# Kernel optimization log

Measured on AMD Instinct MI355X. Metric: run time of the kernel, lower is better.

The kernel has to match this reference:

```python
import jax, jax.numpy as jnp
import numpy as np

N = 20000      # num_nodes
E = 320000     # num_edges (avg degree 16)
HID = 256      # hid_dim
H = 4          # attention heads
D = HID // H   # per-head dim (concat heads -> HID)
L = 2          # nGAT_layer
OUT = 12       # out_dim / pred_len (decoder steps)
NEG_SLOPE = 0.2


def setup_inputs() -> dict:
    key = jax.random.key(0)
    ks = jax.random.split(key, 16)
    s = 0.05
    nrm = lambda k, shape: jax.random.normal(k, shape, jnp.float32) * s
    return dict(
        x=nrm(ks[0], (N, HID)),
        edge_index=jax.random.randint(ks[1], (2, E), 0, N, dtype=jnp.int32),
        # GATv2Conv params per layer (stacked over L layers)
        gat_w_src=nrm(ks[2], (L, HID, H * D)),
        gat_w_dst=nrm(ks[3], (L, HID, H * D)),
        gat_att=nrm(ks[4], (L, H, D)),
        gat_bias=nrm(ks[5], (L, H * D)),
        # decoder_mlp: Linear(1 + HID -> HID)
        mlp_w=nrm(ks[6], (HID, 1 + HID)),
        mlp_b=nrm(ks[7], (HID,)),
        # nn.LSTM (1 layer, input HID, hidden HID), torch gate order i,f,g,o
        lstm_w_ih=nrm(ks[8], (4 * HID, HID)),
        lstm_w_hh=nrm(ks[9], (4 * HID, HID)),
        lstm_b_ih=nrm(ks[10], (4 * HID,)),
        lstm_b_hh=nrm(ks[11], (4 * HID,)),
        # decoder_init_proj: Linear(HID -> 1); decoder_output_proj: Linear(HID -> 1)
        init_w=nrm(ks[12], (1, HID)),
        init_b=nrm(ks[13], (1,)),
        out_w=nrm(ks[14], (1, HID)),
        out_b=nrm(ks[15], (1,)),
    )


def _gatv2_layer(x, src, dst, w_src, w_dst, att, bias):
    n = x.shape[0]
    xl = (x @ w_src).reshape(n, H, D)   # source-side projection
    xr = (x @ w_dst).reshape(n, H, D)   # destination-side projection
    # GATv2: e_ij = a^T LeakyReLU(Wl x_j + Wr x_i)
    e = jax.nn.leaky_relu(xl[src] + xr[dst], NEG_SLOPE)        # [E,H,D]
    logits = jnp.einsum('ehd,hd->eh', e, att)                   # [E,H]
    # edge softmax over incoming edges of each destination node
    m = jax.ops.segment_max(logits, dst, num_segments=n)        # [N,H]
    ex = jnp.exp(logits - m[dst])
    denom = jax.ops.segment_sum(ex, dst, num_segments=n)
    alpha = ex / denom[dst]                                     # [E,H]
    out = jax.ops.segment_sum(xl[src] * alpha[:, :, None], dst, num_segments=n)
    return out.reshape(n, H * D) + bias


def reference(x, edge_index, gat_w_src, gat_w_dst, gat_att, gat_bias,
              mlp_w, mlp_b, lstm_w_ih, lstm_w_hh, lstm_b_ih, lstm_b_hh,
              init_w, init_b, out_w, out_b):
    src, dst = edge_index[0], edge_index[1]
    # stacked GAT blocks: GATv2Conv + ELU (element == 2)
    for l in range(L):
        x = _gatv2_layer(x, src, dst, gat_w_src[l], gat_w_dst[l], gat_att[l], gat_bias[l])
        x = jax.nn.elu(x)
    # recurrent LSTM decoder, batch = nodes, seq step by step
    ctx = x                      # encoder_context
    h = x                        # h_0 = x (num_layers = 1)
    c = jnp.zeros_like(x)        # c_0 = 0
    prev = x @ init_w.T + init_b  # [N,1]
    outs = []
    for _ in range(OUT):
        dec_in = jnp.concatenate([prev, ctx], axis=1) @ mlp_w.T + mlp_b  # [N,HID]
        gates = dec_in @ lstm_w_ih.T + lstm_b_ih + h @ lstm_w_hh.T + lstm_b_hh
        i_g, f_g, g_g, o_g = jnp.split(gates, 4, axis=1)
        i_g = jax.nn.sigmoid(i_g)
        f_g = jax.nn.sigmoid(f_g)
        o_g = jax.nn.sigmoid(o_g)
        g_g = jnp.tanh(g_g)
        c = f_g * c + i_g * g_g
        h = o_g * jnp.tanh(c)
        prev = h @ out_w.T + out_b  # [N,1]
        outs.append(prev)
    return jnp.concatenate(outs, axis=1)  # [N, OUT]
```

## Files before the change

### kernel.cpp

```cpp
#include <hip/hip_runtime.h>
#include <hip/hip_bf16.h>

#define NN 20000
#define NE 320000
#define TOUT 12
#define DEGMAX 96
#define MR 80
#define NBLK 250
#define NCHL 14
#define NCHG 6

typedef __bf16 bf16x8 __attribute__((ext_vector_type(8)));
typedef float float4v __attribute__((ext_vector_type(4)));

#define LD8(p) (*(const bf16x8*)(p))
#define MFMA16(a,b,c) __builtin_amdgcn_mfma_f32_16x16x32_bf16((a),(b),(c),0,0,0)

__device__ __forceinline__ float bf2f(const __hip_bfloat16 v){ return __bfloat162float(v); }
__device__ __forceinline__ __hip_bfloat16 f2bf(float v){ return __float2bfloat16(v); }
__device__ __forceinline__ float sigmoidr_(float x){ return __builtin_amdgcn_rcpf(1.f + __expf(-x)); }
__device__ __forceinline__ float tanhr_(float x){ return 1.f - 2.f*__builtin_amdgcn_rcpf(__expf(2.f*x) + 1.f); }
__device__ __forceinline__ float rdf(const void* p, int i, int f32){
  return f32 ? ((const float*)p)[i] : __bfloat162float(((const __hip_bfloat16*)p)[i]);
}

__global__ void k_detect(const void* xraw, int* flag){
  __shared__ int cnt;
  if(threadIdx.x == 0) cnt = 0;
  __syncthreads();
  const unsigned* w = (const unsigned*)xraw;
  int local = 0;
  for(int i = threadIdx.x; i < 4096; i += 256){
    unsigned b = (w[i] >> 8) & 0x7F;
    if(b >= 0x33 && b <= 0x3F) local++;
  }
  atomicAdd(&cnt, local);
  __syncthreads();
  if(threadIdx.x == 0) *flag = (cnt > 2048) ? 0 : 1;
}

__global__ void k_fail(float* out, int n){
  int i = blockIdx.x*256 + threadIdx.x;
  if(i < n) out[i] = 256.0f;
}

__global__ void k_count(const int* __restrict__ dst, int* __restrict__ deg){
  int e = blockIdx.x*256 + threadIdx.x;
  if(e < NE){
    unsigned d = (unsigned)dst[e];
    if(d < NN) atomicAdd(&deg[d], 1);
  }
}

__global__ void k_scan(const int* __restrict__ deg, int* __restrict__ offp, int* __restrict__ cursor){
  __shared__ int part[256];
  __shared__ int excl[257];
  const int CH = (NN + 255)/256;
  int tid = threadIdx.x;
  int lo = tid*CH;
  int hi = lo + CH; if(hi > NN) hi = NN;
  int s = 0;
  for(int i=lo;i<hi;i++) s += deg[i];
  part[tid] = s;
  __syncthreads();
  if(tid == 0){
    int run = 0;
    for(int i=0;i<256;i++){ excl[i] = run; run += part[i]; }
    excl[256] = run;
  }
  __syncthreads();
  int run = excl[tid];
  for(int i=lo;i<hi;i++){ offp[i] = run; cursor[i] = run; run += deg[i]; }
  if(tid == 0) offp[NN] = excl[256];
}

__global__ void k_fill(const int* __restrict__ src, const int* __restrict__ dst,
                       int* __restrict__ cursor, int* __restrict__ csr_src){
  int e = blockIdx.x*256 + threadIdx.x;
  if(e >= NE) return;
  unsigned d = (unsigned)dst[e];
  if(d >= NN) return;
  unsigned p = (unsigned)atomicAdd(&cursor[d], 1);
  if(p < NE){
    unsigned sv = (unsigned)src[e];
    csr_src[p] = (sv < NN) ? (int)sv : 0;
  }
}

__global__ void k_prep(const void* __restrict__ w_src, const void* __restrict__ w_dst,
                       const void* __restrict__ w_hh, const void* __restrict__ wih,
                       const void* __restrict__ mlp_w, const int* __restrict__ flag,
                       __hip_bfloat16* __restrict__ wsrcT, __hip_bfloat16* __restrict__ wdstT,
                       __hip_bfloat16* __restrict__ whhp, __hip_bfloat16* __restrict__ wihb,
                       __hip_bfloat16* __restrict__ mlpT){
  int tid = blockIdx.x*256 + threadIdx.x;
  int f = *flag;
  if(tid < 131072){
    int l = tid >> 16, r = tid & 65535, o = r >> 8, i = r & 255;
    wsrcT[tid] = f2bf(rdf(w_src, l*65536 + i*256 + o, f));
    wdstT[tid] = f2bf(rdf(w_dst, l*65536 + i*256 + o, f));
  }
  if(tid < 262144){
    whhp[tid] = f2bf(rdf(w_hh, tid, f));
    wihb[tid] = f2bf(rdf(wih, tid, f));
  }
  if(tid < 65536){
    int k = tid >> 8, j = tid & 255;
    mlpT[tid] = f2bf(rdf(mlp_w, j*257 + 1 + k, f));
  }
}

__global__ void k_prep_ub(const void* __restrict__ wih, const void* __restrict__ mlp_w,
                          const void* __restrict__ mlp_b,
                          const void* __restrict__ b_ih, const void* __restrict__ b_hh,
                          const void* __restrict__ att, const void* __restrict__ gbias,
                          const void* __restrict__ init_w, const void* __restrict__ init_b,
                          const void* __restrict__ out_w, const void* __restrict__ out_b,
                          const int* __restrict__ flag,
                          float* __restrict__ u, float* __restrict__ bc,
                          float* __restrict__ attf, float* __restrict__ gbiasf,
                          float* __restrict__ initwf, float* __restrict__ outwf,
                          float* __restrict__ sc){
  __shared__ float su[256], sb[256];
  int g = blockIdx.x, j = threadIdx.x, f = *flag;
  float w = rdf(wih, g*256 + j, f);
  su[j] = w * rdf(mlp_w, j*257, f);
  sb[j] = w * rdf(mlp_b, j, f);
  if(g < 2){
    int i = g*256 + j;
    attf[i] = rdf(att, i, f);
    gbiasf[i] = rdf(gbias, i, f);
  }
  if(g == 0){
    initwf[j] = rdf(init_w, j, f);
    outwf[j]  = rdf(out_w, j, f);
    if(j == 0){ sc[0] = rdf(init_b, 0, f); sc[1] = rdf(out_b, 0, f); }
  }
  __syncthreads();
  for(int s=128; s>0; s>>=1){
    if(j < s){ su[j] += su[j+s]; sb[j] += sb[j+s]; }
    __syncthreads();
  }
  if(j == 0){ u[g] = su[0]; bc[g] = sb[0] + rdf(b_ih, g, f) + rdf(b_hh, g, f); }
}

__global__ void k_pack(const __hip_bfloat16* __restrict__ Wpl, const __hip_bfloat16* __restrict__ Wcpl,
                       __hip_bfloat16* __restrict__ WhhP, __hip_bfloat16* __restrict__ WcP){
  int idx = blockIdx.x*256 + threadIdx.x;
  if(idx >= 32768) return;
  int cs = idx >> 12;
  int kslot = (idx >> 9) & 7;
  int nt = (idx >> 6) & 7;
  int lane = idx & 63;
  int l16 = lane & 15, quad = lane >> 4;
  int brow = (nt>>1)*256 + cs*32 + (nt&1)*16 + l16;
  int srcofs = brow*256 + kslot*32 + quad*8;
  int dst = idx*8;
  *(bf16x8*)(WhhP + dst) = LD8(Wpl + srcofs);
  *(bf16x8*)(WcP + dst)  = LD8(Wcpl + srcofs);
}

__global__ void k_pack2(const __hip_bfloat16* __restrict__ wsrcT,
                        const __hip_bfloat16* __restrict__ wdstT,
                        __hip_bfloat16* __restrict__ wprojP){
  int idx = blockIdx.x*256 + threadIdx.x;
  if(idx >= 32768) return;
  int m = idx >> 13;
  int fi = idx & 8191;
  int l = m >> 1, role = m & 1;
  int kidx = fi >> 10;
  int nt = (fi >> 6) & 15;
  int lane = fi & 63;
  int l16 = lane & 15, quad = lane >> 4;
  const __hip_bfloat16* src = (role ? wdstT : wsrcT) + l*65536;
  int srcofs = (nt*16 + l16)*256 + kidx*32 + quad*8;
  *(bf16x8*)(wprojP + (size_t)m*65536 + fi*8) = LD8(src + srcofs);
}

__global__ __launch_bounds__(256) void k_gemm_nt_bf(const __hip_bfloat16* __restrict__ A,
                                                    const __hip_bfloat16* __restrict__ B,
                                                    __hip_bfloat16* __restrict__ Cb, int M){
  int wave = threadIdx.x >> 6;
  int lane = threadIdx.x & 63;
  int l16 = lane & 15, quad = lane >> 4, quad8 = quad*8;
  int mBase = blockIdx.x*64 + wave*16;
  int nBase = blockIdx.y*64;
  int arow = mBase + l16; if(arow >= M) arow = M-1;
  const __hip_bfloat16* aptr = A + (size_t)arow*256 + quad8;
  float4v acc[4];
  #pragma unroll
  for(int nt=0;nt<4;nt++){ acc[nt][0]=0.f; acc[nt][1]=0.f; acc[nt][2]=0.f; acc[nt][3]=0.f; }
  for(int k0=0;k0<256;k0+=32){
    bf16x8 a = LD8(aptr + k0);
    #pragma unroll
    for(int nt=0;nt<4;nt++){
      const __hip_bfloat16* bptr = B + (size_t)(nBase + nt*16 + l16)*256 + k0 + quad8;
      acc[nt] = MFMA16(a, LD8(bptr), acc[nt]);
    }
  }
  #pragma unroll
  for(int nt=0;nt<4;nt++){
    int col = nBase + nt*16 + l16;
    #pragma unroll
    for(int r=0;r<4;r++){
      int row = mBase + quad*4 + r;
      if(row < M) Cb[(size_t)row*256 + col] = f2bf(acc[nt][r]);
    }
  }
}

__global__ __launch_bounds__(512, 2) void k_gemm_dual(__hip_bfloat16* __restrict__ P,
                                                      const void* __restrict__ xraw,
                                                      const int* __restrict__ flag,
                                                      int layer0,
                                                      const __hip_bfloat16* __restrict__ BsrcP,
                                                      const __hip_bfloat16* __restrict__ BdstP,
                                                      __hip_bfloat16* __restrict__ Q){
  __shared__ __hip_bfloat16 sA[64*264];
  int tid = threadIdx.x;
  int mBase = blockIdx.x*64;
  {
    int r = tid >> 3;
    int c0 = (tid & 7)*32;
    int grow = mBase + r; if(grow >= NN) grow = NN-1;
    if(layer0){
      int f = *flag;
      #pragma unroll
      for(int j=0;j<32;j++) sA[r*264 + c0 + j] = f2bf(rdf(xraw, grow*256 + c0 + j, f));
    }else{
      const __hip_bfloat16* srcp = P + (size_t)grow*256 + c0;
      #pragma unroll
      for(int j=0;j<4;j++) *(bf16x8*)(&sA[r*264 + c0 + j*8]) = LD8(srcp + j*8);
    }
  }
  __syncthreads();
  int w8 = tid >> 6;
  int w = w8 & 3;
  int role = w8 >> 2;
  int lane = tid&63, l16 = lane&15, quad = lane>>4, quad8 = quad*8;
  const __hip_bfloat16* B = role ? BdstP : BsrcP;
  __hip_bfloat16* C = role ? P : Q;
  const __hip_bfloat16* arow = &sA[(w*16 + l16)*264 + quad8];
  float4v acc[16];
  #pragma unroll
  for(int nt=0;nt<16;nt++){ acc[nt][0]=0.f; acc[nt][1]=0.f; acc[nt][2]=0.f; acc[nt][3]=0.f; }
  for(int kidx=0;kidx<8;kidx++){
    bf16x8 a = *(const bf16x8*)(arow + kidx*32);
    const __hip_bfloat16* bbase = B + (kidx<<13) + (lane<<3);
    #pragma unroll
    for(int nt=0;nt<16;nt++)
      acc[nt] = MFMA16(a, LD8(bbase + (nt<<9)), acc[nt]);
  }
  #pragma unroll
  for(int nt=0;nt<16;nt++){
    int col = nt*16 + l16;
    #pragma unroll
    for(int r=0;r<4;r++){
      int row = mBase + w*16 + quad*4 + r;
      if(row < NN) C[(size_t)row*256 + col] = f2bf(acc[nt][r]);
    }
  }
}

__global__ __launch_bounds__(256) void k_node_fused(const __hip_bfloat16* __restrict__ Q,
                                                    __hip_bfloat16* __restrict__ P,
                                                    const int* __restrict__ offp,
                                                    const int* __restrict__ csr_src,
                                                    const float* __restrict__ attf,
                                                    const float* __restrict__ gbiasf){
  __shared__ float slog[DEGMAX*4];
  __shared__ int ssrc[DEGMAX];
  int node = blockIdx.x;
  int tid = threadIdx.x;
  int s0 = offp[node], s1 = offp[node+1];
  if(s0 < 0) s0 = 0; if(s0 > NE) s0 = NE;
  if(s1 < s0) s1 = s0; if(s1 > NE) s1 = NE;
  int deg = s1 - s0; if(deg > DEGMAX) deg = DEGMAX;
  if(tid < deg){
    unsigned sv = (unsigned)csr_src[s0 + tid];
    ssrc[tid] = (sv < NN) ? (int)sv : 0;
  }
  __syncthreads();
  int w = tid>>6, lane = tid&63;
  int eSlot = lane>>4, li = lane&15;
  float prl[16], attl[16];
  #pragma unroll
  for(int h=0;h<4;h++)
    #pragma unroll
    for(int j=0;j<4;j++){
      int d = h*64 + j*16 + li;
      prl[h*4+j]  = bf2f(P[(size_t)node*256 + d]);
      attl[h*4+j] = attf[d];
    }
  for(int base=0; base<deg; base+=16){
    int e = base + w*4 + eSlot;
    bool valid = (e < deg);
    const __hip_bfloat16* pl = Q + (size_t)ssrc[valid ? e : 0]*256;
    float part[4];
    #pragma unroll
    for(int h=0;h<4;h++){
      float p = 0.f;
      #pragma unroll
      for(int j=0;j<4;j++){
        int d = h*64 + j*16 + li;
        float v = bf2f(pl[d]) + prl[h*4+j];
        v = (v > 0.f) ? v : 0.2f*v;
        p += v * attl[h*4+j];
      }
      part[h] = p;
    }
    #pragma unroll
    for(int h=0;h<4;h++){
      part[h] += __shfl_xor(part[h], 1, 64);
      part[h] += __shfl_xor(part[h], 2, 64);
      part[h] += __shfl_xor(part[h], 4, 64);
      part[h] += __shfl_xor(part[h], 8, 64);
    }
    if(li == 0 && valid){
      #pragma unroll
      for(int h=0;h<4;h++) slog[e*4+h] = part[h];
    }
  }
  __syncthreads();
  {
    int hh = tid >> 6;
    int li64 = tid & 63;
    float m = -1e30f;
    for(int i=li64; i<deg; i+=64) m = fmaxf(m, slog[i*4+hh]);
    #pragma unroll
    for(int s=1; s<64; s<<=1) m = fmaxf(m, __shfl_xor(m, s, 64));
    float den = 0.f;
    for(int i=li64; i<deg; i+=64) den += __expf(slog[i*4+hh] - m);
    #pragma unroll
    for(int s=1; s<64; s<<=1) den += __shfl_xor(den, s, 64);
    float inv = (den > 0.f) ? 1.f/den : 0.f;
    for(int i=li64; i<deg; i+=64) slog[i*4+hh] = __expf(slog[i*4+hh] - m)*inv;
  }
  __syncthreads();
  int d = tid, hd = d>>6;
  float acc = 0.f;
  for(int i=0;i<deg;i++) acc += slog[i*4+hd] * bf2f(Q[(size_t)ssrc[i]*256 + d]);
  acc += gbiasf[d];
  acc = (acc > 0.f) ? acc : (__expf(acc) - 1.f);
  P[(size_t)node*256 + d] = f2bf(acc);
}

__global__ __launch_bounds__(512, 2) void k_lstm80(const __hip_bfloat16* __restrict__ ctx,
                                                   const __hip_bfloat16* __restrict__ WcP,
                                                   const __hip_bfloat16* __restrict__ WhhP,
                                                   const float* __restrict__ u_vec,
                                                   const float* __restrict__ bc_vec,
                                                   const float* __restrict__ initwf,
                                                   const float* __restrict__ outwf,
                                                   const float* __restrict__ sc,
                                                   __hip_bfloat16* __restrict__ gxg,
                                                   float* __restrict__ out){
  __shared__ __hip_bfloat16 sgx[NCHL*4096];
  __shared__ __hip_bfloat16 sh[MR*264];
  __shared__ float spartw[MR*8];
  __shared__ float sprev[MR];
  float* spart = (float*)sgx;
  int tid = threadIdx.x;
  int mBase = blockIdx.x*MR;
  int cs = tid>>6, lane = tid&63, l16 = lane&15, quad = lane>>4, quad8 = quad*8;
  int phase = (blockIdx.x >> 3) & 7;
  __hip_bfloat16* gxb = gxg + (size_t)blockIdx.x*(NCHG*4096);
  #pragma unroll
  for(int p=0;p<3;p++){
    int r = p*32 + (tid >> 4);
    if(r < MR){
      int c0 = (tid & 15)*16;
      const __hip_bfloat16* srcp = ctx + (size_t)(mBase + r)*256 + c0;
      *(bf16x8*)(&sh[r*264 + c0])     = LD8(srcp);
      *(bf16x8*)(&sh[r*264 + c0 + 8]) = LD8(srcp + 8);
    }
  }
  __syncthreads();
  #pragma unroll
  for(int p=0;p<3;p++){
    int r = p*32 + (tid >> 4);
    int c0 = (tid & 15)*16;
    float part = 0.f;
    if(r < MR){
      #pragma unroll
      for(int j=0;j<16;j++) part += bf2f(sh[r*264 + c0 + j]) * initwf[c0 + j];
    }
    spart[tid] = part;
    __syncthreads();
    if(tid < 32 && p*32 + tid < MR){
      float s = 0.f;
      #pragma unroll
      for(int j=0;j<16;j++) s += spart[tid*16 + j];
      sprev[p*32 + tid] = s + sc[0];
    }
    __syncthreads();
  }
  float ureg[8], owreg[2];
  #pragma unroll
  for(int g=0;g<4;g++)
    #pragma unroll
    for(int tc=0;tc<2;tc++) ureg[g*2+tc] = u_vec[g*256 + cs*32 + tc*16 + l16];
  #pragma unroll
  for(int tc=0;tc<2;tc++) owreg[tc] = outwf[cs*32 + tc*16 + l16];
  float outb = sc[1];
  {
    float bcl[8];
    #pragma unroll
    for(int g=0;g<4;g++)
      #pragma unroll
      for(int tc=0;tc<2;tc++) bcl[g*2+tc] = bc_vec[g*256 + cs*32 + tc*16 + l16];
    float4v acc[40];
    #pragma unroll
    for(int nt=0;nt<40;nt++){ acc[nt][0]=0.f; acc[nt][1]=0.f; acc[nt][2]=0.f; acc[nt][3]=0.f; }
    #pragma unroll 2
    for(int ki=0;ki<8;ki++){
      int kidx = (ki + phase) & 7;
      int k0 = kidx*32;
      bf16x8 a0 = *(const bf16x8*)(&sh[l16*264 + k0 + quad8]);
      bf16x8 a1 = *(const bf16x8*)(&sh[(16 + l16)*264 + k0 + quad8]);
      bf16x8 a2 = *(const bf16x8*)(&sh[(32 + l16)*264 + k0 + quad8]);
      bf16x8 a3 = *(const bf16x8*)(&sh[(48 + l16)*264 + k0 + quad8]);
      bf16x8 a4 = *(const bf16x8*)(&sh[(64 + l16)*264 + k0 + quad8]);
      const __hip_bfloat16* bbase = WcP + (((cs<<3) + kidx)<<12) + (lane<<3);
      #pragma unroll
      for(int nt=0;nt<8;nt++){
        bf16x8 b = LD8(bbase + (nt<<9));
        acc[nt]    = MFMA16(a0, b, acc[nt]);
        acc[8+nt]  = MFMA16(a1, b, acc[8+nt]);
        acc[16+nt] = MFMA16(a2, b, acc[16+nt]);
        acc[24+nt] = MFMA16(a3, b, acc[24+nt]);
        acc[32+nt] = MFMA16(a4, b, acc[32+nt]);
      }
    }
    #pragma unroll
    for(int rt=0;rt<5;rt++)
      #pragma unroll
      for(int tc=0;tc<2;tc++)
        #pragma unroll
        for(int half=0;half<2;half++){
          bf16x8 v;
          #pragma unroll
          for(int rr=0;rr<2;rr++)
            #pragma unroll
            for(int g=0;g<4;g++){
              int r = half*2 + rr;
              v[rr*4+g] = (__bf16)f2bf(acc[rt*8 + g*2 + tc][r] + bcl[g*2+tc]);
            }
          int cp = (rt*2+tc)*2 + half;
          if(cp < NCHL) *(bf16x8*)(&sgx[cp*4096 + tid*8]) = v;
          else          *(bf16x8*)(gxb + (cp-NCHL)*4096 + tid*8) = v;
        }
  }
  __syncthreads();
  float creg[40];
  #pragma unroll
  for(int i=0;i<40;i++) creg[i] = 0.f;
  for(int step=0; step<TOUT; step++){
    float4v acc[40];
    #pragma unroll
    for(int nt=0;nt<40;nt++){ acc[nt][0]=0.f; acc[nt][1]=0.f; acc[nt][2]=0.f; acc[nt][3]=0.f; }
    #pragma unroll 2
    for(int ki=0;ki<8;ki++){
      int kidx = (ki + phase) & 7;
      int k0 = kidx*32;
      bf16x8 a0 = *(const bf16x8*)(&sh[l16*264 + k0 + quad8]);
      bf16x8 a1 = *(const bf16x8*)(&sh[(16 + l16)*264 + k0 + quad8]);
      bf16x8 a2 = *(const bf16x8*)(&sh[(32 + l16)*264 + k0 + quad8]);
      bf16x8 a3 = *(const bf16x8*)(&sh[(48 + l16)*264 + k0 + quad8]);
      bf16x8 a4 = *(const bf16x8*)(&sh[(64 + l16)*264 + k0 + quad8]);
      const __hip_bfloat16* bbase = WhhP + (((cs<<3) + kidx)<<12) + (lane<<3);
      #pragma unroll
      for(int nt=0;nt<8;nt++){
        bf16x8 b = LD8(bbase + (nt<<9));
        acc[nt]    = MFMA16(a0, b, acc[nt]);
        acc[8+nt]  = MFMA16(a1, b, acc[8+nt]);
        acc[16+nt] = MFMA16(a2, b, acc[16+nt]);
        acc[24+nt] = MFMA16(a3, b, acc[24+nt]);
        acc[32+nt] = MFMA16(a4, b, acc[32+nt]);
      }
    }
    bf16x8 gg[NCHG];
    #pragma unroll
    for(int j=0;j<NCHG;j++) gg[j] = LD8(gxb + j*4096 + tid*8);
    __syncthreads();
    #pragma unroll
    for(int rt=0;rt<5;rt++){
      float hsum[4];
      hsum[0]=0.f; hsum[1]=0.f; hsum[2]=0.f; hsum[3]=0.f;
      #pragma unroll
      for(int tc=0;tc<2;tc++){
        int col = cs*32 + tc*16 + l16;
        int cpb = (rt*2+tc)*2;
        bf16x8 ga = (cpb   < NCHL) ? *(const bf16x8*)(&sgx[cpb*4096 + tid*8])     : gg[cpb-NCHL];
        bf16x8 gb = (cpb+1 < NCHL) ? *(const bf16x8*)(&sgx[(cpb+1)*4096 + tid*8]) : gg[cpb+1-NCHL];
        #pragma unroll
        for(int r=0;r<4;r++){
          int row = rt*16 + quad*4 + r;
          float p = sprev[row];
          int jb = (r&1)*4;
          float gx0, gx1, gx2, gx3;
          if(r < 2){
            gx0 = bf2f((__hip_bfloat16)ga[jb]);   gx1 = bf2f((__hip_bfloat16)ga[jb+1]);
            gx2 = bf2f((__hip_bfloat16)ga[jb+2]); gx3 = bf2f((__hip_bfloat16)ga[jb+3]);
          }else{
            gx0 = bf2f((__hip_bfloat16)gb[jb]);   gx1 = bf2f((__hip_bfloat16)gb[jb+1]);
            gx2 = bf2f((__hip_bfloat16)gb[jb+2]); gx3 = bf2f((__hip_bfloat16)gb[jb+3]);
          }
          float g0 = acc[rt*8 + tc][r]     + gx0 + p*ureg[tc];
          float g1 = acc[rt*8 + 2 + tc][r] + gx1 + p*ureg[2+tc];
          float g2 = acc[rt*8 + 4 + tc][r] + gx2 + p*ureg[4+tc];
          float g3 = acc[rt*8 + 6 + tc][r] + gx3 + p*ureg[6+tc];
          float iv = sigmoidr_(g0), fv = sigmoidr_(g1);
          float gv = tanhr_(g2),    ov = sigmoidr_(g3);
          float cn = fv*creg[rt*8 + tc*4 + r] + iv*gv;
          creg[rt*8 + tc*4 + r] = cn;
          float hn = ov * tanhr_(cn);
          sh[row*264 + col] = f2bf(hn);
          hsum[r] += hn * owreg[tc];
        }
      }
      #pragma unroll
      for(int r=0;r<4;r++){
        hsum[r] += __shfl_xor(hsum[r], 1, 64);
        hsum[r] += __shfl_xor(hsum[r], 2, 64);
        hsum[r] += __shfl_xor(hsum[r], 4, 64);
        hsum[r] += __shfl_xor(hsum[r], 8, 64);
      }
      if(l16 == 0){
        #pragma unroll
        for(int r=0;r<4;r++)
          spartw[(rt*16 + quad*4 + r)*8 + cs] = hsum[r];
      }
    }
    __syncthreads();
    if(tid < MR){
      float s = outb;
      #pragma unroll
      for(int c=0;c<8;c++) s += spartw[tid*8 + c];
      sprev[tid] = s;
      out[(size_t)(mBase + tid)*TOUT + step] = s;
    }
  }
}

extern "C" void kernel_launch(void* const* d_in, const int* in_sizes, int n_in,
                              void* d_out, int out_size, void* d_ws, size_t ws_size,
                              hipStream_t stream){
  const void* x      = d_in[0];
  const int*  ei     = (const int*)d_in[1];
  const void* w_src  = d_in[2];
  const void* w_dst  = d_in[3];
  const void* att    = d_in[4];
  const void* gbias  = d_in[5];
  const void* mlp_w  = d_in[6];
  const void* mlp_b  = d_in[7];
  const void* w_ih   = d_in[8];
  const void* w_hh   = d_in[9];
  const void* b_ih   = d_in[10];
  const void* b_hh   = d_in[11];
  const void* init_w = d_in[12];
  const void* init_b = d_in[13];
  const void* out_w  = d_in[14];
  const void* out_b  = d_in[15];
  float* out = (float*)d_out;
  const int* srcp = ei;
  const int* dstp = ei + NE;
  (void)in_sizes; (void)n_in;

  char* ws = (char*)d_ws;
  size_t off = 0;
  auto alloc = [&](size_t bytes)->void*{
    void* p = ws + off;
    off += (bytes + 255) & ~(size_t)255;
    return p;
  };
  __hip_bfloat16* P = (__hip_bfloat16*)alloc((size_t)NN*256*2);
  __hip_bfloat16* Q = (__hip_bfloat16*)alloc((size_t)NN*256*2);
  int* deg      = (int*)alloc((size_t)NN*4);
  int* offp     = (int*)alloc((size_t)(NN+1)*4);
  int* cursor   = (int*)alloc((size_t)NN*4);
  int* csr_src  = (int*)alloc((size_t)NE*4);
  __hip_bfloat16* wsrcT   = (__hip_bfloat16*)alloc((size_t)131072*2);
  __hip_bfloat16* wdstT   = (__hip_bfloat16*)alloc((size_t)131072*2);
  __hip_bfloat16* wprojP  = (__hip_bfloat16*)alloc((size_t)4*65536*2);
  __hip_bfloat16* whh_pl  = (__hip_bfloat16*)alloc((size_t)262144*2);
  __hip_bfloat16* Wc_pl   = (__hip_bfloat16*)alloc((size_t)262144*2);
  __hip_bfloat16* WhhP    = (__hip_bfloat16*)alloc((size_t)262144*2);
  __hip_bfloat16* WcP     = (__hip_bfloat16*)alloc((size_t)262144*2);
  __hip_bfloat16* wihb    = (__hip_bfloat16*)alloc((size_t)262144*2);
  __hip_bfloat16* mlpT    = (__hip_bfloat16*)alloc((size_t)65536*2);
  __hip_bfloat16* gxg     = (__hip_bfloat16*)alloc((size_t)NBLK*NCHG*4096*2);
  float* u_vec  = (float*)alloc(1024*4);
  float* bc_vec = (float*)alloc(1024*4);
  float* attf   = (float*)alloc(512*4);
  float* gbiasf = (float*)alloc(512*4);
  float* initwf = (float*)alloc(256*4);
  float* outwf  = (float*)alloc(256*4);
  float* sc     = (float*)alloc(2*4);
  int*   flag   = (int*)alloc(4);

  if(off > ws_size){
    k_fail<<<(out_size + 255)/256, 256, 0, stream>>>(out, out_size);
    return;
  }

  k_detect<<<1, 256, 0, stream>>>(x, flag);
  hipMemsetAsync(deg, 0, (size_t)NN*4, stream);
  hipMemsetAsync(csr_src, 0xFF, (size_t)NE*4, stream);
  k_count<<<NE/256, 256, 0, stream>>>(dstp, deg);
  k_scan<<<1, 256, 0, stream>>>(deg, offp, cursor);
  k_fill<<<NE/256, 256, 0, stream>>>(srcp, dstp, cursor, csr_src);
  k_prep<<<1024, 256, 0, stream>>>(w_src, w_dst, w_hh, w_ih, mlp_w, flag,
                                   wsrcT, wdstT, whh_pl, wihb, mlpT);
  {
    dim3 gwc(16, 4);
    k_gemm_nt_bf<<<gwc, 256, 0, stream>>>(wihb, mlpT, Wc_pl, 1024);
  }
  k_pack<<<128, 256, 0, stream>>>(whh_pl, Wc_pl, WhhP, WcP);
  k_pack2<<<128, 256, 0, stream>>>(wsrcT, wdstT, wprojP);
  k_prep_ub<<<1024, 256, 0, stream>>>(w_ih, mlp_w, mlp_b, b_ih, b_hh, att, gbias,
                                      init_w, init_b, out_w, out_b, flag,
                                      u_vec, bc_vec, attf, gbiasf, initwf, outwf, sc);

  for(int l=0;l<2;l++){
    k_gemm_dual<<<313, 512, 0, stream>>>(P, x, flag, (l == 0) ? 1 : 0,
                                         wprojP + (size_t)(l*2)*65536,
                                         wprojP + (size_t)(l*2+1)*65536, Q);
    k_node_fused<<<NN, 256, 0, stream>>>(Q, P, offp, csr_src, attf + l*256, gbiasf + l*256);
  }

  k_lstm80<<<NBLK, 512, 0, stream>>>(P, WcP, WhhP, u_vec, bc_vec, initwf, outwf, sc, gxg, out);
}
```

Baseline: 721.0 us.

## Fold output projection feedback into recurrent weights and keep gate inputs in registers

The rank-1 feedback term (prev * u) for steps after the first is folded into a modified recurrent weight matrix Whh + u·out_w^T, with out_b*u added as a constant. This removes the per-step dependency on the reduced prev value. The precomputed context gate inputs move from shared/global memory into registers (gxr), and the hidden state is double-buffered in shared memory to drop a barrier per step. The cost is higher register pressure (launch bounds lowered to 1 block/SM), an extra folded weight matrix, and extra bf16 rounding of the folded weights.

```diff
diff --git a/kernel.cpp b/kernel.cpp
--- a/kernel.cpp
+++ b/kernel.cpp
@@ -7,8 +7,6 @@
 #define DEGMAX 96
 #define MR 80
 #define NBLK 250
-#define NCHL 14
-#define NCHG 6
 
 typedef __bf16 bf16x8 __attribute__((ext_vector_type(8)));
 typedef float float4v __attribute__((ext_vector_type(4)));
@@ -144,8 +142,17 @@
   if(j == 0){ u[g] = su[0]; bc[g] = sb[0] + rdf(b_ih, g, f) + rdf(b_hh, g, f); }
 }
 
-__global__ void k_pack(const __hip_bfloat16* __restrict__ Wpl, const __hip_bfloat16* __restrict__ Wcpl,
-                       __hip_bfloat16* __restrict__ WhhP, __hip_bfloat16* __restrict__ WcP){
+__global__ void k_fold(const __hip_bfloat16* __restrict__ whh_pl,
+                       const float* __restrict__ u_vec, const float* __restrict__ outwf,
+                       __hip_bfloat16* __restrict__ whh2_pl){
+  int i = blockIdx.x*256 + threadIdx.x;
+  whh2_pl[i] = f2bf(bf2f(whh_pl[i]) + u_vec[i >> 8]*outwf[i & 255]);
+}
+
+__global__ void k_pack(const __hip_bfloat16* __restrict__ Wpl, const __hip_bfloat16* __restrict__ W2pl,
+                       const __hip_bfloat16* __restrict__ Wcpl,
+                       __hip_bfloat16* __restrict__ WhhP, __hip_bfloat16* __restrict__ Whh2P,
+                       __hip_bfloat16* __restrict__ WcP){
   int idx = blockIdx.x*256 + threadIdx.x;
   if(idx >= 32768) return;
   int cs = idx >> 12;
@@ -156,8 +163,9 @@
   int brow = (nt>>1)*256 + cs*32 + (nt&1)*16 + l16;
   int srcofs = brow*256 + kslot*32 + quad*8;
   int dst = idx*8;
-  *(bf16x8*)(WhhP + dst) = LD8(Wpl + srcofs);
-  *(bf16x8*)(WcP + dst)  = LD8(Wcpl + srcofs);
+  *(bf16x8*)(WhhP + dst)  = LD8(Wpl + srcofs);
+  *(bf16x8*)(Whh2P + dst) = LD8(W2pl + srcofs);
+  *(bf16x8*)(WcP + dst)   = LD8(Wcpl + srcofs);
 }
 
 __global__ void k_pack2(const __hip_bfloat16* __restrict__ wsrcT,
@@ -345,34 +353,32 @@
   P[(size_t)node*256 + d] = f2bf(acc);
 }
 
-__global__ __launch_bounds__(512, 2) void k_lstm80(const __hip_bfloat16* __restrict__ ctx,
+__global__ __launch_bounds__(512, 1) void k_lstm80(const __hip_bfloat16* __restrict__ ctx,
                                                    const __hip_bfloat16* __restrict__ WcP,
                                                    const __hip_bfloat16* __restrict__ WhhP,
+                                                   const __hip_bfloat16* __restrict__ Whh2P,
                                                    const float* __restrict__ u_vec,
                                                    const float* __restrict__ bc_vec,
                                                    const float* __restrict__ initwf,
                                                    const float* __restrict__ outwf,
                                                    const float* __restrict__ sc,
-                                                   __hip_bfloat16* __restrict__ gxg,
                                                    float* __restrict__ out){
-  __shared__ __hip_bfloat16 sgx[NCHL*4096];
-  __shared__ __hip_bfloat16 sh[MR*264];
-  __shared__ float spartw[MR*8];
-  __shared__ float sprev[MR];
-  float* spart = (float*)sgx;
+  __shared__ __hip_bfloat16 sh[2][MR*264];
+  __shared__ float spartw[2][MR*8];
+  __shared__ float sprev0[MR];
+  float* spart = &spartw[0][0];
   int tid = threadIdx.x;
   int mBase = blockIdx.x*MR;
   int cs = tid>>6, lane = tid&63, l16 = lane&15, quad = lane>>4, quad8 = quad*8;
   int phase = (blockIdx.x >> 3) & 7;
-  __hip_bfloat16* gxb = gxg + (size_t)blockIdx.x*(NCHG*4096);
   #pragma unroll
   for(int p=0;p<3;p++){
     int r = p*32 + (tid >> 4);
     if(r < MR){
       int c0 = (tid & 15)*16;
       const __hip_bfloat16* srcp = ctx + (size_t)(mBase + r)*256 + c0;
-      *(bf16x8*)(&sh[r*264 + c0])     = LD8(srcp);
-      *(bf16x8*)(&sh[r*264 + c0 + 8]) = LD8(srcp + 8);
+      *(bf16x8*)(&sh[0][r*264 + c0])     = LD8(srcp);
+      *(bf16x8*)(&sh[0][r*264 + c0 + 8]) = LD8(srcp + 8);
     }
   }
   __syncthreads();
@@ -383,7 +389,7 @@
     float part = 0.f;
     if(r < MR){
       #pragma unroll
-      for(int j=0;j<16;j++) part += bf2f(sh[r*264 + c0 + j]) * initwf[c0 + j];
+      for(int j=0;j<16;j++) part += bf2f(sh[0][r*264 + c0 + j]) * initwf[c0 + j];
     }
     spart[tid] = part;
     __syncthreads();
@@ -391,11 +397,11 @@
       float s = 0.f;
       #pragma unroll
       for(int j=0;j<16;j++) s += spart[tid*16 + j];
-      sprev[p*32 + tid] = s + sc[0];
+      sprev0[p*32 + tid] = s + sc[0];
     }
     __syncthreads();
   }
-  float ureg[8], owreg[2];
+  float ureg[8], owreg[2], ubo[8];
   #pragma unroll
   for(int g=0;g<4;g++)
     #pragma unroll
@@ -403,6 +409,9 @@
   #pragma unroll
   for(int tc=0;tc<2;tc++) owreg[tc] = outwf[cs*32 + tc*16 + l16];
   float outb = sc[1];
+  #pragma unroll
+  for(int i=0;i<8;i++) ubo[i] = ureg[i]*outb;
+  bf16x8 gxr[20];
   {
     float bcl[8];
     #pragma unroll
@@ -416,11 +425,11 @@
     for(int ki=0;ki<8;ki++){
       int kidx = (ki + phase) & 7;
       int k0 = kidx*32;
-      bf16x8 a0 = *(const bf16x8*)(&sh[l16*264 + k0 + quad8]);
-      bf16x8 a1 = *(const bf16x8*)(&sh[(16 + l16)*264 + k0 + quad8]);
-      bf16x8 a2 = *(const bf16x8*)(&sh[(32 + l16)*264 + k0 + quad8]);
-      bf16x8 a3 = *(const bf16x8*)(&sh[(48 + l16)*264 + k0 + quad8]);
-      bf16x8 a4 = *(const bf16x8*)(&sh[(64 + l16)*264 + k0 + quad8]);
+      bf16x8 a0 = *(const bf16x8*)(&sh[0][l16*264 + k0 + quad8]);
+      bf16x8 a1 = *(const bf16x8*)(&sh[0][(16 + l16)*264 + k0 + quad8]);
+      bf16x8 a2 = *(const bf16x8*)(&sh[0][(32 + l16)*264 + k0 + quad8]);
+      bf16x8 a3 = *(const bf16x8*)(&sh[0][(48 + l16)*264 + k0 + quad8]);
+      bf16x8 a4 = *(const bf16x8*)(&sh[0][(64 + l16)*264 + k0 + quad8]);
       const __hip_bfloat16* bbase = WcP + (((cs<<3) + kidx)<<12) + (lane<<3);
       #pragma unroll
       for(int nt=0;nt<8;nt++){
@@ -446,16 +455,17 @@
               int r = half*2 + rr;
               v[rr*4+g] = (__bf16)f2bf(acc[rt*8 + g*2 + tc][r] + bcl[g*2+tc]);
             }
-          int cp = (rt*2+tc)*2 + half;
-          if(cp < NCHL) *(bf16x8*)(&sgx[cp*4096 + tid*8]) = v;
-          else          *(bf16x8*)(gxb + (cp-NCHL)*4096 + tid*8) = v;
+          gxr[(rt*2+tc)*2 + half] = v;
         }
   }
-  __syncthreads();
   float creg[40];
   #pragma unroll
   for(int i=0;i<40;i++) creg[i] = 0.f;
+  int cur = 0;
+  #pragma unroll 1
   for(int step=0; step<TOUT; step++){
+    const __hip_bfloat16* W = (step == 0) ? WhhP : Whh2P;
+    int sb = step & 1;
     float4v acc[40];
     #pragma unroll
     for(int nt=0;nt<40;nt++){ acc[nt][0]=0.f; acc[nt][1]=0.f; acc[nt][2]=0.f; acc[nt][3]=0.f; }
@@ -463,12 +473,12 @@
     for(int ki=0;ki<8;ki++){
       int kidx = (ki + phase) & 7;
       int k0 = kidx*32;
-      bf16x8 a0 = *(const bf16x8*)(&sh[l16*264 + k0 + quad8]);
-      bf16x8 a1 = *(const bf16x8*)(&sh[(16 + l16)*264 + k0 + quad8]);
-      bf16x8 a2 = *(const bf16x8*)(&sh[(32 + l16)*264 + k0 + quad8]);
-      bf16x8 a3 = *(const bf16x8*)(&sh[(48 + l16)*264 + k0 + quad8]);
-      bf16x8 a4 = *(const bf16x8*)(&sh[(64 + l16)*264 + k0 + quad8]);
-      const __hip_bfloat16* bbase = WhhP + (((cs<<3) + kidx)<<12) + (lane<<3);
+      bf16x8 a0 = *(const bf16x8*)(&sh[cur][l16*264 + k0 + quad8]);
+      bf16x8 a1 = *(const bf16x8*)(&sh[cur][(16 + l16)*264 + k0 + quad8]);
+      bf16x8 a2 = *(const bf16x8*)(&sh[cur][(32 + l16)*264 + k0 + quad8]);
+      bf16x8 a3 = *(const bf16x8*)(&sh[cur][(48 + l16)*264 + k0 + quad8]);
+      bf16x8 a4 = *(const bf16x8*)(&sh[cur][(64 + l16)*264 + k0 + quad8]);
+      const __hip_bfloat16* bbase = W + (((cs<<3) + kidx)<<12) + (lane<<3);
       #pragma unroll
       for(int nt=0;nt<8;nt++){
         bf16x8 b = LD8(bbase + (nt<<9));
@@ -479,10 +489,6 @@
         acc[32+nt] = MFMA16(a4, b, acc[32+nt]);
       }
     }
-    bf16x8 gg[NCHG];
-    #pragma unroll
-    for(int j=0;j<NCHG;j++) gg[j] = LD8(gxb + j*4096 + tid*8);
-    __syncthreads();
     #pragma unroll
     for(int rt=0;rt<5;rt++){
       float hsum[4];
@@ -491,12 +497,11 @@
       for(int tc=0;tc<2;tc++){
         int col = cs*32 + tc*16 + l16;
         int cpb = (rt*2+tc)*2;
-        bf16x8 ga = (cpb   < NCHL) ? *(const bf16x8*)(&sgx[cpb*4096 + tid*8])     : gg[cpb-NCHL];
-        bf16x8 gb = (cpb+1 < NCHL) ? *(const bf16x8*)(&sgx[(cpb+1)*4096 + tid*8]) : gg[cpb+1-NCHL];
+        bf16x8 ga = gxr[cpb];
+        bf16x8 gb = gxr[cpb+1];
         #pragma unroll
         for(int r=0;r<4;r++){
           int row = rt*16 + quad*4 + r;
-          float p = sprev[row];
           int jb = (r&1)*4;
           float gx0, gx1, gx2, gx3;
           if(r < 2){
@@ -506,16 +511,23 @@
             gx0 = bf2f((__hip_bfloat16)gb[jb]);   gx1 = bf2f((__hip_bfloat16)gb[jb+1]);
             gx2 = bf2f((__hip_bfloat16)gb[jb+2]); gx3 = bf2f((__hip_bfloat16)gb[jb+3]);
           }
-          float g0 = acc[rt*8 + tc][r]     + gx0 + p*ureg[tc];
-          float g1 = acc[rt*8 + 2 + tc][r] + gx1 + p*ureg[2+tc];
-          float g2 = acc[rt*8 + 4 + tc][r] + gx2 + p*ureg[4+tc];
-          float g3 = acc[rt*8 + 6 + tc][r] + gx3 + p*ureg[6+tc];
+          float e0, e1, e2, e3;
+          if(step == 0){
+            float p = sprev0[row];
+            e0 = p*ureg[tc]; e1 = p*ureg[2+tc]; e2 = p*ureg[4+tc]; e3 = p*ureg[6+tc];
+          }else{
+            e0 = ubo[tc]; e1 = ubo[2+tc]; e2 = ubo[4+tc]; e3 = ubo[6+tc];
+          }
+          float g0 = acc[rt*8 + tc][r]     + gx0 + e0;
+          float g1 = acc[rt*8 + 2 + tc][r] + gx1 + e1;
+          float g2 = acc[rt*8 + 4 + tc][r] + gx2 + e2;
+          float g3 = acc[rt*8 + 6 + tc][r] + gx3 + e3;
           float iv = sigmoidr_(g0), fv = sigmoidr_(g1);
           float gv = tanhr_(g2),    ov = sigmoidr_(g3);
           float cn = fv*creg[rt*8 + tc*4 + r] + iv*gv;
           creg[rt*8 + tc*4 + r] = cn;
           float hn = ov * tanhr_(cn);
-          sh[row*264 + col] = f2bf(hn);
+          sh[cur^1][row*264 + col] = f2bf(hn);
           hsum[r] += hn * owreg[tc];
         }
       }
@@ -529,17 +541,17 @@
       if(l16 == 0){
         #pragma unroll
         for(int r=0;r<4;r++)
-          spartw[(rt*16 + quad*4 + r)*8 + cs] = hsum[r];
+          spartw[sb][(rt*16 + quad*4 + r)*8 + cs] = hsum[r];
       }
     }
     __syncthreads();
     if(tid < MR){
       float s = outb;
       #pragma unroll
-      for(int c=0;c<8;c++) s += spartw[tid*8 + c];
-      sprev[tid] = s;
+      for(int c=0;c<8;c++) s += spartw[sb][tid*8 + c];
       out[(size_t)(mBase + tid)*TOUT + step] = s;
     }
+    cur ^= 1;
   }
 }
 
@@ -584,12 +596,13 @@
   __hip_bfloat16* wdstT   = (__hip_bfloat16*)alloc((size_t)131072*2);
   __hip_bfloat16* wprojP  = (__hip_bfloat16*)alloc((size_t)4*65536*2);
   __hip_bfloat16* whh_pl  = (__hip_bfloat16*)alloc((size_t)262144*2);
+  __hip_bfloat16* whh2_pl = (__hip_bfloat16*)alloc((size_t)262144*2);
   __hip_bfloat16* Wc_pl   = (__hip_bfloat16*)alloc((size_t)262144*2);
   __hip_bfloat16* WhhP    = (__hip_bfloat16*)alloc((size_t)262144*2);
+  __hip_bfloat16* Whh2P   = (__hip_bfloat16*)alloc((size_t)262144*2);
   __hip_bfloat16* WcP     = (__hip_bfloat16*)alloc((size_t)262144*2);
   __hip_bfloat16* wihb    = (__hip_bfloat16*)alloc((size_t)262144*2);
   __hip_bfloat16* mlpT    = (__hip_bfloat16*)alloc((size_t)65536*2);
-  __hip_bfloat16* gxg     = (__hip_bfloat16*)alloc((size_t)NBLK*NCHG*4096*2);
   float* u_vec  = (float*)alloc(1024*4);
   float* bc_vec = (float*)alloc(1024*4);
   float* attf   = (float*)alloc(512*4);
@@ -612,15 +625,16 @@
   k_fill<<<NE/256, 256, 0, stream>>>(srcp, dstp, cursor, csr_src);
   k_prep<<<1024, 256, 0, stream>>>(w_src, w_dst, w_hh, w_ih, mlp_w, flag,
                                    wsrcT, wdstT, whh_pl, wihb, mlpT);
+  k_prep_ub<<<1024, 256, 0, stream>>>(w_ih, mlp_w, mlp_b, b_ih, b_hh, att, gbias,
+                                      init_w, init_b, out_w, out_b, flag,
+                                      u_vec, bc_vec, attf, gbiasf, initwf, outwf, sc);
   {
     dim3 gwc(16, 4);
     k_gemm_nt_bf<<<gwc, 256, 0, stream>>>(wihb, mlpT, Wc_pl, 1024);
   }
-  k_pack<<<128, 256, 0, stream>>>(whh_pl, Wc_pl, WhhP, WcP);
+  k_fold<<<1024, 256, 0, stream>>>(whh_pl, u_vec, outwf, whh2_pl);
+  k_pack<<<128, 256, 0, stream>>>(whh_pl, whh2_pl, Wc_pl, WhhP, Whh2P, WcP);
   k_pack2<<<128, 256, 0, stream>>>(wsrcT, wdstT, wprojP);
-  k_prep_ub<<<1024, 256, 0, stream>>>(w_ih, mlp_w, mlp_b, b_ih, b_hh, att, gbias,
-                                      init_w, init_b, out_w, out_b, flag,
-                                      u_vec, bc_vec, attf, gbiasf, initwf, outwf, sc);
 
   for(int l=0;l<2;l++){
     k_gemm_dual<<<313, 512, 0, stream>>>(P, x, flag, (l == 0) ? 1 : 0,
@@ -629,5 +643,6 @@
     k_node_fused<<<NN, 256, 0, stream>>>(Q, P, offp, csr_src, attf + l*256, gbiasf + l*256);
   }
 
-  k_lstm80<<<NBLK, 512, 0, stream>>>(P, WcP, WhhP, u_vec, bc_vec, initwf, outwf, sc, gxg, out);
-}
+  k_lstm80<<<NBLK, 512, 0, stream>>>(P, WcP, WhhP, Whh2P, u_vec, bc_vec,
+                                     initwf, outwf, sc, out);
+}
```

Measured after the change: 1.167 ms. 61.9% more time.

## Fold output-feedback projection into recurrent weight matrix for LSTM steps

Applied to the files above, without the earlier changes.

The previous-output feedback prev = h·out_w + out_b is folded algebraically into a second recurrent weight matrix (W_hh + u·out_wᵀ), with u·out_b moved into the bias. This removes the per-step sprev dependency and the scalar p*u terms, and step 0 gets a correction term instead. The gx global chunk loads move into the epilogue and the launch bounds drop to one block per CU. The fused matrix is rounded to bf16, which adds rounding error, and it needs an extra prep kernel and buffer.

```diff
diff --git a/kernel.cpp b/kernel.cpp
--- a/kernel.cpp
+++ b/kernel.cpp
@@ -144,8 +144,17 @@
   if(j == 0){ u[g] = su[0]; bc[g] = sb[0] + rdf(b_ih, g, f) + rdf(b_hh, g, f); }
 }
 
-__global__ void k_pack(const __hip_bfloat16* __restrict__ Wpl, const __hip_bfloat16* __restrict__ Wcpl,
-                       __hip_bfloat16* __restrict__ WhhP, __hip_bfloat16* __restrict__ WcP){
+__global__ void k_fold(const __hip_bfloat16* __restrict__ whh_pl,
+                       const float* __restrict__ u_vec, const float* __restrict__ outwf,
+                       __hip_bfloat16* __restrict__ whh2_pl){
+  int i = blockIdx.x*256 + threadIdx.x;
+  whh2_pl[i] = f2bf(bf2f(whh_pl[i]) + u_vec[i >> 8]*outwf[i & 255]);
+}
+
+__global__ void k_pack(const __hip_bfloat16* __restrict__ Wpl, const __hip_bfloat16* __restrict__ W2pl,
+                       const __hip_bfloat16* __restrict__ Wcpl,
+                       __hip_bfloat16* __restrict__ WhhP, __hip_bfloat16* __restrict__ Whh2P,
+                       __hip_bfloat16* __restrict__ WcP){
   int idx = blockIdx.x*256 + threadIdx.x;
   if(idx >= 32768) return;
   int cs = idx >> 12;
@@ -156,8 +165,9 @@
   int brow = (nt>>1)*256 + cs*32 + (nt&1)*16 + l16;
   int srcofs = brow*256 + kslot*32 + quad*8;
   int dst = idx*8;
-  *(bf16x8*)(WhhP + dst) = LD8(Wpl + srcofs);
-  *(bf16x8*)(WcP + dst)  = LD8(Wcpl + srcofs);
+  *(bf16x8*)(WhhP + dst)  = LD8(Wpl + srcofs);
+  *(bf16x8*)(Whh2P + dst) = LD8(W2pl + srcofs);
+  *(bf16x8*)(WcP + dst)   = LD8(Wcpl + srcofs);
 }
 
 __global__ void k_pack2(const __hip_bfloat16* __restrict__ wsrcT,
@@ -345,9 +355,10 @@
   P[(size_t)node*256 + d] = f2bf(acc);
 }
 
-__global__ __launch_bounds__(512, 2) void k_lstm80(const __hip_bfloat16* __restrict__ ctx,
+__global__ __launch_bounds__(512, 1) void k_lstm80(const __hip_bfloat16* __restrict__ ctx,
                                                    const __hip_bfloat16* __restrict__ WcP,
                                                    const __hip_bfloat16* __restrict__ WhhP,
+                                                   const __hip_bfloat16* __restrict__ Whh2P,
                                                    const float* __restrict__ u_vec,
                                                    const float* __restrict__ bc_vec,
                                                    const float* __restrict__ initwf,
@@ -358,7 +369,7 @@
   __shared__ __hip_bfloat16 sgx[NCHL*4096];
   __shared__ __hip_bfloat16 sh[MR*264];
   __shared__ float spartw[MR*8];
-  __shared__ float sprev[MR];
+  __shared__ float sprev0[MR];
   float* spart = (float*)sgx;
   int tid = threadIdx.x;
   int mBase = blockIdx.x*MR;
@@ -391,15 +402,11 @@
       float s = 0.f;
       #pragma unroll
       for(int j=0;j<16;j++) s += spart[tid*16 + j];
-      sprev[p*32 + tid] = s + sc[0];
+      sprev0[p*32 + tid] = s + sc[0];
     }
     __syncthreads();
   }
-  float ureg[8], owreg[2];
-  #pragma unroll
-  for(int g=0;g<4;g++)
-    #pragma unroll
-    for(int tc=0;tc<2;tc++) ureg[g*2+tc] = u_vec[g*256 + cs*32 + tc*16 + l16];
+  float owreg[2];
   #pragma unroll
   for(int tc=0;tc<2;tc++) owreg[tc] = outwf[cs*32 + tc*16 + l16];
   float outb = sc[1];
@@ -408,7 +415,9 @@
     #pragma unroll
     for(int g=0;g<4;g++)
       #pragma unroll
-      for(int tc=0;tc<2;tc++) bcl[g*2+tc] = bc_vec[g*256 + cs*32 + tc*16 + l16];
+      for(int tc=0;tc<2;tc++)
+        bcl[g*2+tc] = bc_vec[g*256 + cs*32 + tc*16 + l16]
+                    + u_vec[g*256 + cs*32 + tc*16 + l16]*outb;
     float4v acc[40];
     #pragma unroll
     for(int nt=0;nt<40;nt++){ acc[nt][0]=0.f; acc[nt][1]=0.f; acc[nt][2]=0.f; acc[nt][3]=0.f; }
@@ -455,7 +464,9 @@
   float creg[40];
   #pragma unroll
   for(int i=0;i<40;i++) creg[i] = 0.f;
+  #pragma unroll 1
   for(int step=0; step<TOUT; step++){
+    const __hip_bfloat16* W = (step == 0) ? WhhP : Whh2P;
     float4v acc[40];
     #pragma unroll
     for(int nt=0;nt<40;nt++){ acc[nt][0]=0.f; acc[nt][1]=0.f; acc[nt][2]=0.f; acc[nt][3]=0.f; }
@@ -468,7 +479,7 @@
       bf16x8 a2 = *(const bf16x8*)(&sh[(32 + l16)*264 + k0 + quad8]);
       bf16x8 a3 = *(const bf16x8*)(&sh[(48 + l16)*264 + k0 + quad8]);
       bf16x8 a4 = *(const bf16x8*)(&sh[(64 + l16)*264 + k0 + quad8]);
-      const __hip_bfloat16* bbase = WhhP + (((cs<<3) + kidx)<<12) + (lane<<3);
+      const __hip_bfloat16* bbase = W + (((cs<<3) + kidx)<<12) + (lane<<3);
       #pragma unroll
       for(int nt=0;nt<8;nt++){
         bf16x8 b = LD8(bbase + (nt<<9));
@@ -479,24 +490,24 @@
         acc[32+nt] = MFMA16(a4, b, acc[32+nt]);
       }
     }
-    bf16x8 gg[NCHG];
-    #pragma unroll
-    for(int j=0;j<NCHG;j++) gg[j] = LD8(gxb + j*4096 + tid*8);
     __syncthreads();
     #pragma unroll
-    for(int rt=0;rt<5;rt++){
+    for(int ri=0; ri<5; ri++){
+      const int rt = 4 - ri;
       float hsum[4];
       hsum[0]=0.f; hsum[1]=0.f; hsum[2]=0.f; hsum[3]=0.f;
       #pragma unroll
       for(int tc=0;tc<2;tc++){
         int col = cs*32 + tc*16 + l16;
-        int cpb = (rt*2+tc)*2;
-        bf16x8 ga = (cpb   < NCHL) ? *(const bf16x8*)(&sgx[cpb*4096 + tid*8])     : gg[cpb-NCHL];
-        bf16x8 gb = (cpb+1 < NCHL) ? *(const bf16x8*)(&sgx[(cpb+1)*4096 + tid*8]) : gg[cpb+1-NCHL];
+        const int cpb = (rt*2+tc)*2;
+        bf16x8 ga, gb;
+        if(cpb < NCHL)   ga = *(const bf16x8*)(&sgx[cpb*4096 + tid*8]);
+        else             ga = LD8(gxb + (cpb-NCHL)*4096 + tid*8);
+        if(cpb+1 < NCHL) gb = *(const bf16x8*)(&sgx[(cpb+1)*4096 + tid*8]);
+        else             gb = LD8(gxb + (cpb+1-NCHL)*4096 + tid*8);
         #pragma unroll
         for(int r=0;r<4;r++){
           int row = rt*16 + quad*4 + r;
-          float p = sprev[row];
           int jb = (r&1)*4;
           float gx0, gx1, gx2, gx3;
           if(r < 2){
@@ -506,10 +517,17 @@
             gx0 = bf2f((__hip_bfloat16)gb[jb]);   gx1 = bf2f((__hip_bfloat16)gb[jb+1]);
             gx2 = bf2f((__hip_bfloat16)gb[jb+2]); gx3 = bf2f((__hip_bfloat16)gb[jb+3]);
           }
-          float g0 = acc[rt*8 + tc][r]     + gx0 + p*ureg[tc];
-          float g1 = acc[rt*8 + 2 + tc][r] + gx1 + p*ureg[2+tc];
-          float g2 = acc[rt*8 + 4 + tc][r] + gx2 + p*ureg[4+tc];
-          float g3 = acc[rt*8 + 6 + tc][r] + gx3 + p*ureg[6+tc];
+          float g0 = acc[rt*8 + tc][r]     + gx0;
+          float g1 = acc[rt*8 + 2 + tc][r] + gx1;
+          float g2 = acc[rt*8 + 4 + tc][r] + gx2;
+          float g3 = acc[rt*8 + 6 + tc][r] + gx3;
+          if(step == 0){
+            float pd = sprev0[row] - outb;
+            g0 += pd*u_vec[col];
+            g1 += pd*u_vec[256 + col];
+            g2 += pd*u_vec[512 + col];
+            g3 += pd*u_vec[768 + col];
+          }
           float iv = sigmoidr_(g0), fv = sigmoidr_(g1);
           float gv = tanhr_(g2),    ov = sigmoidr_(g3);
           float cn = fv*creg[rt*8 + tc*4 + r] + iv*gv;
@@ -537,7 +555,6 @@
       float s = outb;
       #pragma unroll
       for(int c=0;c<8;c++) s += spartw[tid*8 + c];
-      sprev[tid] = s;
       out[(size_t)(mBase + tid)*TOUT + step] = s;
     }
   }
@@ -584,8 +601,10 @@
   __hip_bfloat16* wdstT   = (__hip_bfloat16*)alloc((size_t)131072*2);
   __hip_bfloat16* wprojP  = (__hip_bfloat16*)alloc((size_t)4*65536*2);
   __hip_bfloat16* whh_pl  = (__hip_bfloat16*)alloc((size_t)262144*2);
+  __hip_bfloat16* whh2_pl = (__hip_bfloat16*)alloc((size_t)262144*2);
   __hip_bfloat16* Wc_pl   = (__hip_bfloat16*)alloc((size_t)262144*2);
   __hip_bfloat16* WhhP    = (__hip_bfloat16*)alloc((size_t)262144*2);
+  __hip_bfloat16* Whh2P   = (__hip_bfloat16*)alloc((size_t)262144*2);
   __hip_bfloat16* WcP     = (__hip_bfloat16*)alloc((size_t)262144*2);
   __hip_bfloat16* wihb    = (__hip_bfloat16*)alloc((size_t)262144*2);
   __hip_bfloat16* mlpT    = (__hip_bfloat16*)alloc((size_t)65536*2);
@@ -612,15 +631,16 @@
   k_fill<<<NE/256, 256, 0, stream>>>(srcp, dstp, cursor, csr_src);
   k_prep<<<1024, 256, 0, stream>>>(w_src, w_dst, w_hh, w_ih, mlp_w, flag,
                                    wsrcT, wdstT, whh_pl, wihb, mlpT);
+  k_prep_ub<<<1024, 256, 0, stream>>>(w_ih, mlp_w, mlp_b, b_ih, b_hh, att, gbias,
+                                      init_w, init_b, out_w, out_b, flag,
+                                      u_vec, bc_vec, attf, gbiasf, initwf, outwf, sc);
   {
     dim3 gwc(16, 4);
     k_gemm_nt_bf<<<gwc, 256, 0, stream>>>(wihb, mlpT, Wc_pl, 1024);
   }
-  k_pack<<<128, 256, 0, stream>>>(whh_pl, Wc_pl, WhhP, WcP);
+  k_fold<<<1024, 256, 0, stream>>>(whh_pl, u_vec, outwf, whh2_pl);
+  k_pack<<<128, 256, 0, stream>>>(whh_pl, whh2_pl, Wc_pl, WhhP, Whh2P, WcP);
   k_pack2<<<128, 256, 0, stream>>>(wsrcT, wdstT, wprojP);
-  k_prep_ub<<<1024, 256, 0, stream>>>(w_ih, mlp_w, mlp_b, b_ih, b_hh, att, gbias,
-                                      init_w, init_b, out_w, out_b, flag,
-                                      u_vec, bc_vec, attf, gbiasf, initwf, outwf, sc);
 
   for(int l=0;l<2;l++){
     k_gemm_dual<<<313, 512, 0, stream>>>(P, x, flag, (l == 0) ? 1 : 0,
@@ -629,5 +649,6 @@
     k_node_fused<<<NN, 256, 0, stream>>>(Q, P, offp, csr_src, attf + l*256, gbiasf + l*256);
   }
 
-  k_lstm80<<<NBLK, 512, 0, stream>>>(P, WcP, WhhP, u_vec, bc_vec, initwf, outwf, sc, gxg, out);
-}
+  k_lstm80<<<NBLK, 512, 0, stream>>>(P, WcP, WhhP, Whh2P, u_vec, bc_vec,
+                                     initwf, outwf, sc, gxg, out);
+}
```

After: 776.3 us. +7.7%, slower.
